# Performance work log

Measured on AMD Instinct MI355X. Metric: run time of the kernel, lower is better.

Reference implementation:

```python
import jax, jax.numpy as jnp
import numpy as np
from jax.ops import segment_sum

N_NODES = 100000
N_EDGES = 1600000

def setup_inputs() -> dict:
    key = jax.random.key(0)
    ks = jax.random.split(key, 16)
    s = 0.1
    return {
        "x": jax.random.normal(ks[0], (N_NODES, 8), jnp.float32),
        "edge_index": jax.random.randint(ks[1], (2, N_EDGES), 0, N_NODES, jnp.int32),
        "W1l": jax.random.normal(ks[2], (8, 128)) * s,
        "W1r": jax.random.normal(ks[3], (8, 128)) * s,
        "b1": jnp.zeros((128,)),
        "W2l": jax.random.normal(ks[4], (128, 128)) * s,
        "W2r": jax.random.normal(ks[5], (128, 128)) * s,
        "b2": jnp.zeros((128,)),
        "W3l": jax.random.normal(ks[6], (128, 1)) * s,
        "W3r": jax.random.normal(ks[7], (128, 1)) * s,
        "b3": jnp.zeros((1,)),
        "Ta1_W": jax.random.normal(ks[8], (4, 8, 8)) * s,
        "Ta1_b": jnp.zeros((8,)),
        "Ta2_W": jax.random.normal(ks[9], (4, 8, 1)) * s,
        "Ta2_b": jnp.zeros((1,)),
        "Tb1_W": jax.random.normal(ks[10], (10, 8, 8)) * s,
        "Tb1_b": jnp.zeros((8,)),
        "Tb2_W": jax.random.normal(ks[11], (10, 8, 1)) * s,
        "Tb2_b": jnp.zeros((1,)),
        "lin2_W": jax.random.normal(ks[12], (2, 1)) * s,
        "lin2_b": jnp.zeros((1,)),
        "lin1_W": jax.random.normal(ks[13], (2, 1)) * s,
        "lin1_b": jnp.zeros((1,)),
    }

def reference(x, edge_index, W1l, W1r, b1, W2l, W2r, b2, W3l, W3r, b3,
              Ta1_W, Ta1_b, Ta2_W, Ta2_b, Tb1_W, Tb1_b, Tb2_W, Tb2_b,
              lin2_W, lin2_b, lin1_W, lin1_b):
    N = x.shape[0]
    src, dst = edge_index[0], edge_index[1]  # message flows src -> dst

    # in-degree of each target node (edge weight = 1)
    deg = segment_sum(jnp.ones_like(src, dtype=x.dtype), dst, num_segments=N)

    # --- SAGEConv: lin_l(mean_{j in N(i)} x_j) + lin_r(x_i) + bias ---
    inv_deg = jnp.where(deg > 0, 1.0 / jnp.maximum(deg, 1.0), 0.0)
    def sage(h, Wl, Wr, b):
        agg = segment_sum(h[src], dst, num_segments=N) * inv_deg[:, None]
        return agg @ Wl + h @ Wr + b

    # --- TAGConv: sym-normalized adjacency powers, no self loops ---
    dinv = jnp.where(deg > 0, jax.lax.rsqrt(jnp.maximum(deg, 1.0)), 0.0)
    norm = dinv[src] * dinv[dst]  # [E]
    def tag(h, Ws, b):  # Ws: [K+1, in, out]
        out = h @ Ws[0]
        for k in range(1, Ws.shape[0]):
            h = segment_sum(h[src] * norm[:, None], dst, num_segments=N)
            out = out + h @ Ws[k]
        return out + b

    relu = jax.nn.relu
    x1 = relu(sage(x, W1l, W1r, b1))
    x1 = relu(sage(x1, W2l, W2r, b2))
    x1 = relu(sage(x1, W3l, W3r, b3))

    x2 = relu(tag(x, Ta1_W, Ta1_b))
    x2 = relu(tag(x2, Ta2_W, Ta2_b))

    x3 = relu(tag(x, Tb1_W, Tb1_b))
    x3 = relu(tag(x3, Tb2_W, Tb2_b))

    x23 = relu(jnp.concatenate([x2, x3], axis=1) @ lin2_W + lin2_b)
    out = relu(jnp.concatenate([x1, x23], axis=1) @ lin1_W + lin1_b)
    return out
```

## Files before the change

### kernel.cpp

```cpp
#include <hip/hip_runtime.h>

#define NN 100000
#define NE 1600000
#define TPB 256

__global__ void k_init(int* __restrict__ deg, int* __restrict__ cursor, int* __restrict__ counter) {
    int i = blockIdx.x * TPB + threadIdx.x;
    if (i < NN) { deg[i] = 0; cursor[i] = 0; }
    if (i == 0) counter[0] = 0;
}

__global__ void k_deg(const int* __restrict__ dst, int* __restrict__ deg) {
    int e = blockIdx.x * TPB + threadIdx.x;
    if (e < NE) atomicAdd(&deg[dst[e]], 1);
}

__global__ void k_prep(const int* __restrict__ deg, float* __restrict__ inv_deg,
                       float* __restrict__ dinv, int* __restrict__ row_start,
                       int* __restrict__ counter) {
    int i = blockIdx.x * TPB + threadIdx.x;
    int lane = threadIdx.x & 63;
    int d = (i < NN) ? deg[i] : 0;
    int incl = d;
    #pragma unroll
    for (int o = 1; o < 64; o <<= 1) {
        int v = __shfl_up(incl, o, 64);
        if (lane >= o) incl += v;
    }
    int total = __shfl(incl, 63, 64);
    int base = 0;
    if (lane == 63) base = atomicAdd(counter, total);
    base = __shfl(base, 63, 64);
    if (i < NN) {
        row_start[i] = base + incl - d;
        inv_deg[i] = d > 0 ? 1.0f / (float)d : 0.0f;
        dinv[i]    = d > 0 ? 1.0f / sqrtf((float)d) : 0.0f;
    }
}

__global__ void k_fill(const int* __restrict__ src, const int* __restrict__ dst,
                       const int* __restrict__ row_start, int* __restrict__ cursor,
                       int* __restrict__ col) {
    int e = blockIdx.x * TPB + threadIdx.x;
    if (e < NE) {
        int d = dst[e];
        int p = atomicAdd(&cursor[d], 1);
        col[row_start[d] + p] = src[e];
    }
}

__global__ void k_meanprop8(const float* __restrict__ h, const int* __restrict__ row_start,
                            const int* __restrict__ deg, const float* __restrict__ inv_deg,
                            const int* __restrict__ col, float* __restrict__ out) {
    int t = blockIdx.x * TPB + threadIdx.x;
    if (t >= NN * 2) return;
    int n = t >> 1, half = t & 1;
    int rs = row_start[n], end = rs + deg[n];
    const float4* h4 = (const float4*)h;
    float4 s0 = make_float4(0,0,0,0), s1 = make_float4(0,0,0,0);
    int e = rs + half;
    for (; e + 2 < end; e += 4) {
        int c0 = col[e] * 2, c1 = col[e + 2] * 2;
        float4 a0 = h4[c0], a1 = h4[c0 + 1], b0 = h4[c1], b1 = h4[c1 + 1];
        s0.x += a0.x + b0.x; s0.y += a0.y + b0.y; s0.z += a0.z + b0.z; s0.w += a0.w + b0.w;
        s1.x += a1.x + b1.x; s1.y += a1.y + b1.y; s1.z += a1.z + b1.z; s1.w += a1.w + b1.w;
    }
    if (e < end) {
        int c0 = col[e] * 2;
        float4 a0 = h4[c0], a1 = h4[c0 + 1];
        s0.x += a0.x; s0.y += a0.y; s0.z += a0.z; s0.w += a0.w;
        s1.x += a1.x; s1.y += a1.y; s1.z += a1.z; s1.w += a1.w;
    }
    s0.x += __shfl_xor(s0.x, 1, 64); s0.y += __shfl_xor(s0.y, 1, 64);
    s0.z += __shfl_xor(s0.z, 1, 64); s0.w += __shfl_xor(s0.w, 1, 64);
    s1.x += __shfl_xor(s1.x, 1, 64); s1.y += __shfl_xor(s1.y, 1, 64);
    s1.z += __shfl_xor(s1.z, 1, 64); s1.w += __shfl_xor(s1.w, 1, 64);
    float w = inv_deg[n];
    float4 o = (half == 0) ? s0 : s1;
    o.x *= w; o.y *= w; o.z *= w; o.w *= w;
    ((float4*)out)[n * 2 + half] = o;
}

__global__ void k_meanprop128(const float* __restrict__ h, const int* __restrict__ row_start,
                              const int* __restrict__ deg, const float* __restrict__ inv_deg,
                              const int* __restrict__ col, float* __restrict__ out) {
    int t = blockIdx.x * TPB + threadIdx.x;
    if (t >= NN * 32) return;
    int n = t >> 5, f4 = t & 31;
    int rs = row_start[n], end = rs + deg[n];
    const float4* h4 = (const float4*)h;
    float4 s = make_float4(0.f, 0.f, 0.f, 0.f);
    int e = rs;
    for (; e + 1 < end; e += 2) {
        float4 v0 = h4[(size_t)col[e] * 32 + f4];
        float4 v1 = h4[(size_t)col[e + 1] * 32 + f4];
        s.x += v0.x + v1.x; s.y += v0.y + v1.y;
        s.z += v0.z + v1.z; s.w += v0.w + v1.w;
    }
    if (e < end) {
        float4 v = h4[(size_t)col[e] * 32 + f4];
        s.x += v.x; s.y += v.y; s.z += v.z; s.w += v.w;
    }
    float w = inv_deg[n];
    s.x *= w; s.y *= w; s.z *= w; s.w *= w;
    ((float4*)out)[t] = s;
}

__global__ void k_tagstep(const float* __restrict__ q, const int* __restrict__ row_start,
                          const int* __restrict__ deg, const float* __restrict__ dinv,
                          const int* __restrict__ col, float* __restrict__ qout,
                          const float* __restrict__ Wa, const float* __restrict__ Wb,
                          float* __restrict__ outa, float* __restrict__ outb,
                          const float* __restrict__ ba, const float* __restrict__ bb,
                          int fina, int finb) {
    int t = blockIdx.x * TPB + threadIdx.x;
    if (t >= NN * 8) return;
    int n = t >> 3, qd = t & 7;
    int half = qd & 1, epar = qd >> 1;
    int rs = row_start[n], end = rs + deg[n];
    const float4* q4 = (const float4*)q;
    float4 s = make_float4(0,0,0,0);
    int e = rs + epar;
    for (; e + 4 < end; e += 8) {
        int c0 = col[e] * 2 + half, c1 = col[e + 4] * 2 + half;
        float4 a = q4[c0], b = q4[c1];
        s.x += a.x + b.x; s.y += a.y + b.y; s.z += a.z + b.z; s.w += a.w + b.w;
    }
    if (e < end) {
        float4 a = q4[col[e] * 2 + half];
        s.x += a.x; s.y += a.y; s.z += a.z; s.w += a.w;
    }
    #pragma unroll
    for (int o = 2; o < 8; o <<= 1) {
        s.x += __shfl_xor(s.x, o, 64); s.y += __shfl_xor(s.y, o, 64);
        s.z += __shfl_xor(s.z, o, 64); s.w += __shfl_xor(s.w, o, 64);
    }
    float dn = dinv[n];
    float m0 = s.x * dn, m1 = s.y * dn, m2 = s.z * dn, m3 = s.w * dn;
    if (qout && epar == 0) {
        ((float4*)qout)[n * 2 + half] = make_float4(m0 * dn, m1 * dn, m2 * dn, m3 * dn);
    }
    float o0 = __shfl_xor(m0, 1, 64), o1 = __shfl_xor(m1, 1, 64);
    float o2 = __shfl_xor(m2, 1, 64), o3 = __shfl_xor(m3, 1, 64);
    float h[8];
    if (half) {
        h[0] = o0; h[1] = o1; h[2] = o2; h[3] = o3;
        h[4] = m0; h[5] = m1; h[6] = m2; h[7] = m3;
    } else {
        h[0] = m0; h[1] = m1; h[2] = m2; h[3] = m3;
        h[4] = o0; h[5] = o1; h[6] = o2; h[7] = o3;
    }
    int f = qd;
    if (Wa) {
        float v = outa[(size_t)n * 8 + f];
        #pragma unroll
        for (int j = 0; j < 8; ++j) v += h[j] * Wa[j * 8 + f];
        if (fina) v = fmaxf(v + ba[f], 0.f);
        outa[(size_t)n * 8 + f] = v;
    }
    {
        float v = outb[(size_t)n * 8 + f];
        #pragma unroll
        for (int j = 0; j < 8; ++j) v += h[j] * Wb[j * 8 + f];
        if (finb) v = fmaxf(v + bb[f], 0.f);
        outb[(size_t)n * 8 + f] = v;
    }
}

__global__ void k_symprop1n(const float* __restrict__ qin, const float* __restrict__ yk,
                            const int* __restrict__ row_start, const int* __restrict__ deg,
                            const float* __restrict__ dinv, const int* __restrict__ col,
                            float* __restrict__ qout, int qstride) {
    int t = blockIdx.x * TPB + threadIdx.x;
    if (t >= NN * 8) return;
    int n = t >> 3, qd = t & 7;
    int rs = row_start[n], d = deg[n];
    float s = 0.f;
    for (int e = rs + qd; e < rs + d; e += 8) s += qin[col[e]];
    s += __shfl_xor(s, 1, 64);
    s += __shfl_xor(s, 2, 64);
    s += __shfl_xor(s, 4, 64);
    if (qd == 0) {
        float dn = dinv[n];
        qout[(size_t)n * qstride] = dn * (dn * s + yk[n]);
    }
}

__global__ void k_symprop2(const float* __restrict__ q2in, const float* __restrict__ yka,
                           const float* __restrict__ ykb, const int* __restrict__ row_start,
                           const int* __restrict__ deg, const float* __restrict__ dinv,
                           const int* __restrict__ col, float* __restrict__ q2out) {
    int t = blockIdx.x * TPB + threadIdx.x;
    if (t >= NN * 8) return;
    int n = t >> 3, qd = t & 7;
    int rs = row_start[n], d = deg[n];
    const float2* q2 = (const float2*)q2in;
    float sa = 0.f, sb = 0.f;
    for (int e = rs + qd; e < rs + d; e += 8) {
        float2 v = q2[col[e]];
        sa += v.x; sb += v.y;
    }
    sa += __shfl_xor(sa, 1, 64); sa += __shfl_xor(sa, 2, 64); sa += __shfl_xor(sa, 4, 64);
    sb += __shfl_xor(sb, 1, 64); sb += __shfl_xor(sb, 2, 64); sb += __shfl_xor(sb, 4, 64);
    if (qd == 0) {
        float dn = dinv[n];
        ((float2*)q2out)[n] = make_float2(dn * (dn * sa + yka[n]),
                                          dn * (dn * sb + ykb[n]));
    }
}

__global__ void k_symprop2fin(const float* __restrict__ q2in, const float* __restrict__ yka,
                              const float* __restrict__ ykb, const int* __restrict__ row_start,
                              const int* __restrict__ deg, const float* __restrict__ dinv,
                              const int* __restrict__ col,
                              const float* __restrict__ biasa, const float* __restrict__ biasb,
                              const float* __restrict__ x1f,
                              const float* __restrict__ l2w, const float* __restrict__ l2b,
                              const float* __restrict__ l1w, const float* __restrict__ l1b,
                              float* __restrict__ out) {
    int t = blockIdx.x * TPB + threadIdx.x;
    if (t >= NN * 8) return;
    int n = t >> 3, qd = t & 7;
    int rs = row_start[n], d = deg[n];
    const float2* q2 = (const float2*)q2in;
    float sa = 0.f, sb = 0.f;
    for (int e = rs + qd; e < rs + d; e += 8) {
        float2 v = q2[col[e]];
        sa += v.x; sb += v.y;
    }
    sa += __shfl_xor(sa, 1, 64); sa += __shfl_xor(sa, 2, 64); sa += __shfl_xor(sa, 4, 64);
    sb += __shfl_xor(sb, 1, 64); sb += __shfl_xor(sb, 2, 64); sb += __shfl_xor(sb, 4, 64);
    if (qd == 0) {
        float dn = dinv[n];
        float x2 = fmaxf(dn * sa + yka[n] + biasa[0], 0.f);
        float x3 = fmaxf(dn * sb + ykb[n] + biasb[0], 0.f);
        float x23 = fmaxf(x2 * l2w[0] + x3 * l2w[1] + l2b[0], 0.f);
        out[n] = fmaxf(x1f[n] * l1w[0] + x23 * l1w[1] + l1b[0], 0.f);
    }
}

__global__ void k_red8(const float* __restrict__ ylp, const float* __restrict__ yrp,
                       float* __restrict__ yl, float* __restrict__ yr) {
    int n = blockIdx.x * TPB + threadIdx.x;
    if (n >= NN) return;
    float sl = 0.f, sr = 0.f;
    #pragma unroll
    for (int j = 0; j < 8; ++j) {
        sl += ylp[(size_t)j * NN + n];
        sr += yrp[(size_t)j * NN + n];
    }
    yl[n] = sl;
    yr[n] = sr;
}

__global__ void k_sage3(const float* __restrict__ yl, const float* __restrict__ yr,
                        const int* __restrict__ row_start, const int* __restrict__ deg,
                        const float* __restrict__ inv_deg, const int* __restrict__ col,
                        const float* __restrict__ b3, float* __restrict__ x1f) {
    int t = blockIdx.x * TPB + threadIdx.x;
    if (t >= NN * 8) return;
    int n = t >> 3, q = t & 7;
    int rs = row_start[n], d = deg[n];
    float s = 0.f;
    for (int e = rs + q; e < rs + d; e += 8) s += yl[col[e]];
    s += __shfl_xor(s, 1, 64);
    s += __shfl_xor(s, 2, 64);
    s += __shfl_xor(s, 4, 64);
    if (q == 0) x1f[n] = fmaxf(s * inv_deg[n] + yr[n] + b3[0], 0.f);
}

__global__ void k_sage1(const float* __restrict__ a8, const float* __restrict__ x,
                        const float* __restrict__ W1l, const float* __restrict__ W1r,
                        const float* __restrict__ b1, float* __restrict__ x1) {
    int t = blockIdx.x * TPB + threadIdx.x;
    if (t >= NN * 16) return;
    int n = t >> 4, og = (t & 15) * 8;
    float acc[8];
    #pragma unroll
    for (int j = 0; j < 8; ++j) acc[j] = b1[og + j];
    const float* ar = a8 + (size_t)n * 8;
    const float* xr = x + (size_t)n * 8;
    #pragma unroll
    for (int k = 0; k < 8; ++k) {
        float av = ar[k], xv = xr[k];
        const float4* wl = (const float4*)(W1l + k * 128 + og);
        const float4* wr = (const float4*)(W1r + k * 128 + og);
        float4 l0 = wl[0], l1 = wl[1], r0 = wr[0], r1 = wr[1];
        acc[0] += av * l0.x + xv * r0.x;
        acc[1] += av * l0.y + xv * r0.y;
        acc[2] += av * l0.z + xv * r0.z;
        acc[3] += av * l0.w + xv * r0.w;
        acc[4] += av * l1.x + xv * r1.x;
        acc[5] += av * l1.y + xv * r1.y;
        acc[6] += av * l1.z + xv * r1.z;
        acc[7] += av * l1.w + xv * r1.w;
    }
    #pragma unroll
    for (int j = 0; j < 8; ++j)
        x1[(size_t)n * 128 + og + j] = fmaxf(acc[j], 0.f);
}

__global__ __launch_bounds__(256) void k_transpose(const float* __restrict__ in0,
        float* __restrict__ out0, const float* __restrict__ in1, float* __restrict__ out1) {
    const float* in = blockIdx.y ? in1 : in0;
    float* outp = blockIdx.y ? out1 : out0;
    __shared__ float t[128][65];
    int n0 = blockIdx.x * 64;
    int tid = threadIdx.x;
    #pragma unroll
    for (int i = 0; i < 8; ++i) {
        int idx = tid + i * 256;
        int nl = idx >> 5;
        int kq = (idx & 31) << 2;
        int n = n0 + nl;
        float4 v = (n < NN) ? *(const float4*)(in + (size_t)n * 128 + kq)
                            : make_float4(0.f, 0.f, 0.f, 0.f);
        t[kq][nl] = v.x; t[kq + 1][nl] = v.y; t[kq + 2][nl] = v.z; t[kq + 3][nl] = v.w;
    }
    __syncthreads();
    #pragma unroll
    for (int i = 0; i < 8; ++i) {
        int idx = tid + i * 256;
        int k = idx >> 4;
        int nq = (idx & 15) << 2;
        if (n0 + nq + 3 < NN) {
            float4 v = make_float4(t[k][nq], t[k][nq + 1], t[k][nq + 2], t[k][nq + 3]);
            *(float4*)(outp + (size_t)k * NN + n0 + nq) = v;
        }
    }
}

__global__ __launch_bounds__(256) void k_sage2f(const float* __restrict__ aT,
        const float* __restrict__ xT, const float* __restrict__ W2l,
        const float* __restrict__ W2r, const float* __restrict__ b2,
        const float* __restrict__ W3l, const float* __restrict__ W3r,
        float* __restrict__ ylp, float* __restrict__ yrp) {
    int xcd = blockIdx.x & 7;
    int s = blockIdx.x >> 3;
    int xblk = xcd * 49 + (s >> 3);
    int ogq = s & 7;
    int og = ogq * 16;
    int n0 = xblk * 256 + threadIdx.x;
    int n = (n0 < NN) ? n0 : (NN - 1);
    float acc[16];
    #pragma unroll
    for (int j = 0; j < 16; ++j) acc[j] = b2[og + j];
    const float* ap = aT + n;
    const float* xp = xT + n;
    const float* wlp = W2l + og;
    const float* wrp = W2r + og;
    #pragma unroll 4
    for (int k = 0; k < 128; ++k) {
        float a = ap[0], xv = xp[0];
        ap += NN; xp += NN;
        const float4* wl4 = (const float4*)(wlp + (k << 7));
        const float4* wr4 = (const float4*)(wrp + (k << 7));
        #pragma unroll
        for (int q = 0; q < 4; ++q) {
            float4 wl = wl4[q], wr = wr4[q];
            acc[q * 4 + 0] += a * wl.x + xv * wr.x;
            acc[q * 4 + 1] += a * wl.y + xv * wr.y;
            acc[q * 4 + 2] += a * wl.z + xv * wr.z;
            acc[q * 4 + 3] += a * wl.w + xv * wr.w;
        }
    }
    float pl = 0.f, pr = 0.f;
    #pragma unroll
    for (int j = 0; j < 16; ++j) {
        float v = fmaxf(acc[j], 0.f);
        pl += v * W3l[og + j];
        pr += v * W3r[og + j];
    }
    if (n0 < NN) {
        ylp[(size_t)ogq * NN + n0] = pl;
        yrp[(size_t)ogq * NN + n0] = pr;
    }
}

__global__ void k_taginit(const float* __restrict__ x, const float* __restrict__ TaW,
                          const float* __restrict__ TbW, const float* __restrict__ dinv,
                          float* __restrict__ outa, float* __restrict__ outb,
                          float* __restrict__ q0) {
    int t = blockIdx.x * TPB + threadIdx.x;
    if (t >= NN * 8) return;
    int n = t >> 3, o = t & 7;
    const float* xr = x + (size_t)n * 8;
    float sa = 0.f, sb = 0.f;
    #pragma unroll
    for (int j = 0; j < 8; ++j) {
        float v = xr[j];
        sa += v * TaW[j * 8 + o];
        sb += v * TbW[j * 8 + o];
    }
    outa[t] = sa;
    outb[t] = sb;
    q0[t] = xr[o] * dinv[n];
}

__global__ void k_tag2projAB(const float* __restrict__ outa, const float* __restrict__ outb,
                             const float* __restrict__ TaW2, const float* __restrict__ TbW2,
                             float* __restrict__ ya, float* __restrict__ yb,
                             const float* __restrict__ dinv,
                             float* __restrict__ q2a, float* __restrict__ qb0) {
    int n = blockIdx.x * TPB + threadIdx.x;
    if (n >= NN) return;
    float dn = dinv[n];
    float ha[8], hb[8];
    #pragma unroll
    for (int j = 0; j < 8; ++j) ha[j] = outa[(size_t)n * 8 + j];
    #pragma unroll
    for (int j = 0; j < 8; ++j) hb[j] = outb[(size_t)n * 8 + j];
    #pragma unroll
    for (int k = 0; k < 4; ++k) {
        float s = 0.f;
        #pragma unroll
        for (int j = 0; j < 8; ++j) s += ha[j] * TaW2[k * 8 + j];
        if (k == 3) q2a[(size_t)n * 2] = s * dn;
        else        ya[(size_t)k * NN + n] = s;
    }
    #pragma unroll
    for (int k = 0; k < 10; ++k) {
        float s = 0.f;
        #pragma unroll
        for (int j = 0; j < 8; ++j) s += hb[j] * TbW2[k * 8 + j];
        if (k == 9) qb0[n] = s * dn;
        else        yb[(size_t)k * NN + n] = s;
    }
}

#define GL(kern, n, ...) \
    kern<<<dim3((unsigned)(((long)(n) + TPB - 1) / TPB)), dim3(TPB), 0, stream>>>(__VA_ARGS__)

extern "C" void kernel_launch(void* const* d_in, const int* in_sizes, int n_in,
                              void* d_out, int out_size, void* d_ws, size_t ws_size,
                              hipStream_t stream) {
    (void)in_sizes; (void)n_in; (void)out_size; (void)ws_size;
    const float* x   = (const float*)d_in[0];
    const int*   ei  = (const int*)d_in[1];
    const int*   src = ei;
    const int*   dst = ei + NE;
    const float* W1l = (const float*)d_in[2];
    const float* W1r = (const float*)d_in[3];
    const float* b1  = (const float*)d_in[4];
    const float* W2l = (const float*)d_in[5];
    const float* W2r = (const float*)d_in[6];
    const float* b2  = (const float*)d_in[7];
    const float* W3l = (const float*)d_in[8];
    const float* W3r = (const float*)d_in[9];
    const float* b3  = (const float*)d_in[10];
    const float* TaW1 = (const float*)d_in[11];
    const float* TaB1 = (const float*)d_in[12];
    const float* TaW2 = (const float*)d_in[13];
    const float* TaB2 = (const float*)d_in[14];
    const float* TbW1 = (const float*)d_in[15];
    const float* TbB1 = (const float*)d_in[16];
    const float* TbW2 = (const float*)d_in[17];
    const float* TbB2 = (const float*)d_in[18];
    const float* l2w = (const float*)d_in[19];
    const float* l2b = (const float*)d_in[20];
    const float* l1w = (const float*)d_in[21];
    const float* l1b = (const float*)d_in[22];
    float* out = (float*)d_out;

    char* p = (char*)d_ws;
    size_t off = 0;
    auto alloc = [&](size_t bytes) -> void* {
        void* r = p + off;
        off = (off + bytes + 255) & ~(size_t)255;
        return r;
    };
    int*   deg       = (int*)  alloc((size_t)NN * 4);
    float* inv_deg   = (float*)alloc((size_t)NN * 4);
    float* dinv      = (float*)alloc((size_t)NN * 4);
    int*   row_start = (int*)  alloc((size_t)NN * 4);
    int*   cursor    = (int*)  alloc((size_t)NN * 4);
    int*   counter   = (int*)  alloc(256);
    int*   col       = (int*)  alloc((size_t)NE * 4);
    float* a8        = (float*)alloc((size_t)NN * 8 * 4);
    float* qA        = (float*)alloc((size_t)NN * 8 * 4);
    float* qB        = (float*)alloc((size_t)NN * 8 * 4);
    float* outa      = (float*)alloc((size_t)NN * 8 * 4);
    float* outb      = (float*)alloc((size_t)NN * 8 * 4);
    float* x1        = (float*)alloc((size_t)NN * 128 * 4);
    float* a128      = (float*)alloc((size_t)NN * 128 * 4);
    float* a128T     = (float*)alloc((size_t)NN * 128 * 4);
    float* x1T       = (float*)alloc((size_t)NN * 128 * 4);
    float* ylp       = (float*)alloc((size_t)NN * 8 * 4);
    float* yrp       = (float*)alloc((size_t)NN * 8 * 4);
    float* yl        = (float*)alloc((size_t)NN * 4);
    float* yr        = (float*)alloc((size_t)NN * 4);
    float* x1f       = (float*)alloc((size_t)NN * 4);
    float* tA        = (float*)alloc((size_t)NN * 4);
    float* tB        = (float*)alloc((size_t)NN * 4);
    float* qb0       = (float*)alloc((size_t)NN * 4);
    float* q2a       = (float*)alloc((size_t)NN * 8);
    float* q2b       = (float*)alloc((size_t)NN * 8);
    float* ya        = (float*)alloc((size_t)NN * 4 * 4);
    float* yb        = (float*)alloc((size_t)NN * 10 * 4);

    GL(k_init, NN, deg, cursor, counter);
    GL(k_deg, NE, dst, deg);
    GL(k_prep, NN, deg, inv_deg, dinv, row_start, counter);
    GL(k_fill, NE, src, dst, row_start, cursor, col);

    GL(k_meanprop8, (long)NN * 2, x, row_start, deg, inv_deg, col, a8);
    GL(k_sage1, (long)NN * 16, a8, x, W1l, W1r, b1, x1);
    GL(k_meanprop128, (long)NN * 32, x1, row_start, deg, inv_deg, col, a128);
    k_transpose<<<dim3((NN + 63) / 64, 2), dim3(256), 0, stream>>>(a128, a128T, x1, x1T);
    k_sage2f<<<dim3(3136), dim3(256), 0, stream>>>(a128T, x1T, W2l, W2r, b2, W3l, W3r, ylp, yrp);
    GL(k_red8, NN, ylp, yrp, yl, yr);
    GL(k_sage3, (long)NN * 8, yl, yr, row_start, deg, inv_deg, col, b3, x1f);

    GL(k_taginit, (long)NN * 8, x, TaW1, TbW1, dinv, outa, outb, qA);
    {
        float* qcur = qA;
        float* qnext = qB;
        for (int k = 1; k <= 9; ++k) {
            float* qout = (k < 9) ? qnext : nullptr;
            const float* Wa = (k <= 3) ? (TaW1 + (size_t)k * 64) : nullptr;
            GL(k_tagstep, (long)NN * 8, qcur, row_start, deg, dinv, col, qout,
               Wa, TbW1 + (size_t)k * 64, outa, outb, TaB1, TbB1,
               (k == 3) ? 1 : 0, (k == 9) ? 1 : 0);
            if (qout) { float* tmp = qcur; qcur = qnext; qnext = tmp; }
        }
    }

    GL(k_tag2projAB, NN, outa, outb, TaW2, TbW2, ya, yb, dinv, q2a, qb0);

    GL(k_symprop1n, (long)NN * 8, qb0, yb + 8 * NN, row_start, deg, dinv, col, tA, 1);
    GL(k_symprop1n, (long)NN * 8, tA,  yb + 7 * NN, row_start, deg, dinv, col, tB, 1);
    GL(k_symprop1n, (long)NN * 8, tB,  yb + 6 * NN, row_start, deg, dinv, col, tA, 1);
    GL(k_symprop1n, (long)NN * 8, tA,  yb + 5 * NN, row_start, deg, dinv, col, tB, 1);
    GL(k_symprop1n, (long)NN * 8, tB,  yb + 4 * NN, row_start, deg, dinv, col, tA, 1);
    GL(k_symprop1n, (long)NN * 8, tA,  yb + 3 * NN, row_start, deg, dinv, col, q2a + 1, 2);

    GL(k_symprop2, (long)NN * 8, q2a, ya + 2 * NN, yb + 2 * NN, row_start, deg, dinv, col, q2b);
    GL(k_symprop2, (long)NN * 8, q2b, ya + 1 * NN, yb + 1 * NN, row_start, deg, dinv, col, q2a);
    GL(k_symprop2fin, (long)NN * 8, q2a, ya + 0 * NN, yb + 0 * NN, row_start, deg, dinv, col,
       TaB2, TbB2, x1f, l2w, l2b, l1w, l1b, out);
}
```

Baseline: 765.9 us.

## Emit transposed x1 directly from sage1, unroll gather and sage2 loops

k_sage1 now uses a 2D grid with one node per thread and writes both the row-major x1 (as float4 stores) and a transposed x1T copy. This removes the x1 half of the transpose kernel, which now only transposes a128. meanprop128 is unrolled to four edges per iteration to raise memory-level parallelism, and sage2f walks its weight pointers incrementally with a deeper unroll. The transposed writes from sage1 are strided per thread but coalesced across a wavefront. The k_sage1 grid change also alters its memory access pattern.

Result: no change. 758.8 us (-0.9%).

```diff
diff --git a/kernel.cpp b/kernel.cpp
--- a/kernel.cpp
+++ b/kernel.cpp
@@ -91,13 +91,17 @@
     const float4* h4 = (const float4*)h;
     float4 s = make_float4(0.f, 0.f, 0.f, 0.f);
     int e = rs;
-    for (; e + 1 < end; e += 2) {
+    for (; e + 3 < end; e += 4) {
         float4 v0 = h4[(size_t)col[e] * 32 + f4];
         float4 v1 = h4[(size_t)col[e + 1] * 32 + f4];
-        s.x += v0.x + v1.x; s.y += v0.y + v1.y;
-        s.z += v0.z + v1.z; s.w += v0.w + v1.w;
-    }
-    if (e < end) {
+        float4 v2 = h4[(size_t)col[e + 2] * 32 + f4];
+        float4 v3 = h4[(size_t)col[e + 3] * 32 + f4];
+        s.x += (v0.x + v1.x) + (v2.x + v3.x);
+        s.y += (v0.y + v1.y) + (v2.y + v3.y);
+        s.z += (v0.z + v1.z) + (v2.z + v3.z);
+        s.w += (v0.w + v1.w) + (v2.w + v3.w);
+    }
+    for (; e < end; ++e) {
         float4 v = h4[(size_t)col[e] * 32 + f4];
         s.x += v.x; s.y += v.y; s.z += v.z; s.w += v.w;
     }
@@ -269,17 +273,19 @@
     if (q == 0) x1f[n] = fmaxf(s * inv_deg[n] + yr[n] + b3[0], 0.f);
 }
 
-__global__ void k_sage1(const float* __restrict__ a8, const float* __restrict__ x,
+__global__ __launch_bounds__(256) void k_sage1(const float* __restrict__ a8,
+                        const float* __restrict__ x,
                         const float* __restrict__ W1l, const float* __restrict__ W1r,
-                        const float* __restrict__ b1, float* __restrict__ x1) {
-    int t = blockIdx.x * TPB + threadIdx.x;
-    if (t >= NN * 16) return;
-    int n = t >> 4, og = (t & 15) * 8;
+                        const float* __restrict__ b1, float* __restrict__ x1,
+                        float* __restrict__ x1T) {
+    int n = blockIdx.x * 256 + threadIdx.x;
+    int og = blockIdx.y * 8;
+    int nc = (n < NN) ? n : (NN - 1);
     float acc[8];
     #pragma unroll
     for (int j = 0; j < 8; ++j) acc[j] = b1[og + j];
-    const float* ar = a8 + (size_t)n * 8;
-    const float* xr = x + (size_t)n * 8;
+    const float* ar = a8 + (size_t)nc * 8;
+    const float* xr = x + (size_t)nc * 8;
     #pragma unroll
     for (int k = 0; k < 8; ++k) {
         float av = ar[k], xv = xr[k];
@@ -295,15 +301,19 @@
         acc[6] += av * l1.z + xv * r1.z;
         acc[7] += av * l1.w + xv * r1.w;
     }
-    #pragma unroll
-    for (int j = 0; j < 8; ++j)
-        x1[(size_t)n * 128 + og + j] = fmaxf(acc[j], 0.f);
-}
-
-__global__ __launch_bounds__(256) void k_transpose(const float* __restrict__ in0,
-        float* __restrict__ out0, const float* __restrict__ in1, float* __restrict__ out1) {
-    const float* in = blockIdx.y ? in1 : in0;
-    float* outp = blockIdx.y ? out1 : out0;
+    if (n < NN) {
+        #pragma unroll
+        for (int j = 0; j < 8; ++j) acc[j] = fmaxf(acc[j], 0.f);
+        *(float4*)(x1 + (size_t)n * 128 + og)     = make_float4(acc[0], acc[1], acc[2], acc[3]);
+        *(float4*)(x1 + (size_t)n * 128 + og + 4) = make_float4(acc[4], acc[5], acc[6], acc[7]);
+        #pragma unroll
+        for (int j = 0; j < 8; ++j)
+            x1T[(size_t)(og + j) * NN + n] = acc[j];
+    }
+}
+
+__global__ __launch_bounds__(256) void k_transpose(const float* __restrict__ in,
+        float* __restrict__ outp) {
     __shared__ float t[128][65];
     int n0 = blockIdx.x * 64;
     int tid = threadIdx.x;
@@ -347,14 +357,12 @@
     for (int j = 0; j < 16; ++j) acc[j] = b2[og + j];
     const float* ap = aT + n;
     const float* xp = xT + n;
-    const float* wlp = W2l + og;
-    const float* wrp = W2r + og;
-    #pragma unroll 4
+    const float4* wl4 = (const float4*)(W2l + og);
+    const float4* wr4 = (const float4*)(W2r + og);
+    #pragma unroll 8
     for (int k = 0; k < 128; ++k) {
         float a = ap[0], xv = xp[0];
         ap += NN; xp += NN;
-        const float4* wl4 = (const float4*)(wlp + (k << 7));
-        const float4* wr4 = (const float4*)(wrp + (k << 7));
         #pragma unroll
         for (int q = 0; q < 4; ++q) {
             float4 wl = wl4[q], wr = wr4[q];
@@ -363,6 +371,7 @@
             acc[q * 4 + 2] += a * wl.z + xv * wr.z;
             acc[q * 4 + 3] += a * wl.w + xv * wr.w;
         }
+        wl4 += 32; wr4 += 32;
     }
     float pl = 0.f, pr = 0.f;
     #pragma unroll
@@ -504,9 +513,9 @@
     GL(k_fill, NE, src, dst, row_start, cursor, col);
 
     GL(k_meanprop8, (long)NN * 2, x, row_start, deg, inv_deg, col, a8);
-    GL(k_sage1, (long)NN * 16, a8, x, W1l, W1r, b1, x1);
+    k_sage1<<<dim3((NN + 255) / 256, 16), dim3(256), 0, stream>>>(a8, x, W1l, W1r, b1, x1, x1T);
     GL(k_meanprop128, (long)NN * 32, x1, row_start, deg, inv_deg, col, a128);
-    k_transpose<<<dim3((NN + 63) / 64, 2), dim3(256), 0, stream>>>(a128, a128T, x1, x1T);
+    k_transpose<<<dim3((NN + 63) / 64), dim3(256), 0, stream>>>(a128, a128T);
     k_sage2f<<<dim3(3136), dim3(256), 0, stream>>>(a128T, x1T, W2l, W2r, b2, W3l, W3r, ylp, yrp);
     GL(k_red8, NN, ylp, yrp, yl, yr);
     GL(k_sage3, (long)NN * 8, yl, yr, row_start, deg, inv_deg, col, b3, x1f);
```
